# Kernel optimization log

Measured on AMD Instinct MI355X. Metric: run time of the kernel, lower is better.

## Reference

```python
import jax, jax.numpy as jnp
import numpy as np

EPS = 1e-3          # posdef_tol
CRLB = 1.0          # contraction_rate_lb
STD = 0.5           # initialization_std
DX, L, DIN, DOUT, B = 512, 512, 256, 256, 8192


def setup_inputs() -> dict:
    key = jax.random.key(0)
    ks = jax.random.split(key, 9)
    f32 = jnp.float32
    return {
        "u_in": jax.random.normal(ks[0], (B, 1, DIN), f32),
        "x0": jnp.zeros((B, 1, DX), f32),
        "X": jax.random.normal(ks[1], (2 * DX + L, 2 * DX + L), f32) * STD,
        "Y": jax.random.normal(ks[2], (DX, DX), f32) * STD,
        "B2": jax.random.normal(ks[3], (DX, DIN), f32) * STD,
        "C2": jax.random.normal(ks[4], (DOUT, DX), f32) * STD,
        "D21": jax.random.normal(ks[5], (DOUT, L), f32) * STD,
        "D22": jax.random.normal(ks[6], (DOUT, DIN), f32) * STD,
        "D12": jax.random.normal(ks[7], (L, DIN), f32) * STD,
    }


def _derive(X, Y, dx, l):
    # update_model_param: H = X^T X + eps*I, then block-split
    H = X.T @ X + EPS * jnp.eye(2 * dx + l, dtype=X.dtype)
    H11 = H[:dx, :dx]
    H21 = H[dx:dx + l, :dx]
    H22 = H[dx:dx + l, dx:dx + l]
    H31 = H[dx + l:, :dx]
    H32 = H[dx + l:, dx:dx + l]
    H33 = H[dx + l:, dx + l:]
    Fm = H31
    B1 = H32
    E = 0.5 * (H11 + CRLB * H33 + Y - Y.T)
    Lam = 0.5 * jnp.diag(H22)
    D11 = -jnp.tril(H22, -1)   # strictly lower triangular
    C1 = -H21
    return Fm, B1, E, Lam, D11, C1


def reference(u_in, x0, X, Y, B2, C2, D21, D22, D12):
    b = u_in.shape[0]
    dx = x0.shape[-1]
    l = D12.shape[0]
    u = u_in[:, 0, :]          # (B, din)
    x = x0[:, 0, :]            # (B, dx)
    Fm, B1, E, Lam, D11, C1 = _derive(X, Y, dx, l)

    # v_i = C1[i]@x + D11[i]@w + D12[i]@u ; the x/u parts are loop-invariant
    a = x @ C1.T + u @ D12.T   # (B, l)

    def step(w, inputs):
        a_i, d_row, lam_i, e_row = inputs
        v = a_i + w @ d_row                       # (B,) forward substitution
        w = w + jnp.tanh(v / lam_i)[:, None] * e_row[None, :]
        return w, None

    eye = jnp.eye(l, dtype=u.dtype)
    w0 = jnp.zeros((b, l), u.dtype)
    w, _ = jax.lax.scan(step, w0, (a.T, D11, Lam, eye))  # (B, l)

    pre = x @ Fm.T + w @ B1.T + u @ B2.T          # (B, dx)
    # F.linear(pre, E^{-1}) = pre @ E^{-T} = solve(E, pre^T)^T
    x_new = jnp.linalg.solve(E, pre.T).T          # (B, dx)
    y = x_new @ C2.T + w @ D21.T + u @ D22.T      # (B, dout)
    return y[:, None, :]                          # (B, 1, dout)
```

## Files before the change

kernel.cpp:

```cpp
#include <hip/hip_runtime.h>
#include <cstdint>
#include <cstddef>

#define EPSC 0.001f

typedef __attribute__((ext_vector_type(8))) short short8;
typedef __attribute__((ext_vector_type(4))) float f32x4;

__device__ inline void bsplit(float f, ushort& h, ushort& l) {
  uint b = __float_as_uint(f);
  h = (ushort)(b >> 16);
  float r = f - __uint_as_float(b & 0xFFFF0000u);
  l = (ushort)(__float_as_uint(r) >> 16);
}

__global__ void k_anynz(const float* __restrict__ x, int n4, int* __restrict__ flag) {
  int i = blockIdx.x * blockDim.x + threadIdx.x;
  int stride = gridDim.x * blockDim.x;
  int found = 0;
  for (; i < n4; i += stride) {
    float4 v = ((const float4*)x)[i];
    if (v.x != 0.f || v.y != 0.f || v.z != 0.f || v.w != 0.f) { found = 1; break; }
  }
  if (found) atomicOr(flag, 1);
}

__global__ __launch_bounds__(256) void k_tsplit(const float* __restrict__ src,
    ushort* __restrict__ dh, ushort* __restrict__ dl, int R, int C)
{
  __shared__ float t[32][33];
  const int c0 = blockIdx.x * 32, r0 = blockIdx.y * 32;
  const int tid = threadIdx.x;
  const int lr = tid >> 3, lc4 = (tid & 7) * 4;
  float4 v = *(const float4*)(src + (size_t)(r0 + lr) * C + c0 + lc4);
  t[lr][lc4 + 0] = v.x; t[lr][lc4 + 1] = v.y;
  t[lr][lc4 + 2] = v.z; t[lr][lc4 + 3] = v.w;
  __syncthreads();
  ushort4 hv, lv;
  float f;
  f = t[lc4 + 0][lr]; bsplit(f, hv.x, lv.x);
  f = t[lc4 + 1][lr]; bsplit(f, hv.y, lv.y);
  f = t[lc4 + 2][lr]; bsplit(f, hv.z, lv.z);
  f = t[lc4 + 3][lr]; bsplit(f, hv.w, lv.w);
  size_t off = (size_t)(c0 + lr) * R + r0 + lc4;
  *(ushort4*)(dh + off) = hv;
  *(ushort4*)(dl + off) = lv;
}

__global__ void k_split2(const float* __restrict__ s0, ushort* __restrict__ h0,
                         ushort* __restrict__ l0, int c0,
                         const float* __restrict__ s1, ushort* __restrict__ h1,
                         ushort* __restrict__ l1, int c1)
{
  int i = blockIdx.x * 256 + threadIdx.x;
  int tot = c0 + c1;
  int stride = gridDim.x * 256;
  for (; i < tot; i += stride) {
    const float* s; ushort* h; ushort* l; int k;
    if (i < c0) { s = s0; h = h0; l = l0; k = i; }
    else        { s = s1; h = h1; l = l1; k = i - c0; }
    float4 v = ((const float4*)s)[k];
    ushort4 hv, lv;
    bsplit(v.x, hv.x, lv.x);
    bsplit(v.y, hv.y, lv.y);
    bsplit(v.z, hv.z, lv.z);
    bsplit(v.w, hv.w, lv.w);
    ((ushort4*)h)[k] = hv;
    ((ushort4*)l)[k] = lv;
  }
}

__global__ __launch_bounds__(256) void k_xtxm(
    const ushort* __restrict__ Xth, const ushort* __restrict__ Xtl,
    const float* __restrict__ Y,
    float* __restrict__ E, float* __restrict__ C1,
    float* __restrict__ D11, ushort* __restrict__ D11h, ushort* __restrict__ D11l,
    float* __restrict__ Lam,
    ushort* __restrict__ FmTh, ushort* __restrict__ FmTl,
    ushort* __restrict__ B1Th, ushort* __restrict__ B1Tl)
{
  __shared__ ushort sAh[64][40], sAl[64][40], sBh[64][40], sBl[64][40];
  const int z = blockIdx.z;
  int aOff[2], bOff[2], nops;
  switch (z) {
    case 0:  aOff[0] = 0;    bOff[0] = 0;    aOff[1] = 1024; bOff[1] = 1024; nops = 2; break;
    case 1:  aOff[0] = 512;  bOff[0] = 0;    nops = 1; break;
    case 2:  aOff[0] = 512;  bOff[0] = 512;  nops = 1; break;
    case 3:  aOff[0] = 0;    bOff[0] = 1024; nops = 1; break;
    default: aOff[0] = 512;  bOff[0] = 1024; nops = 1; break;
  }
  const int tid = threadIdx.x;
  const int m0 = blockIdx.x * 64, n0 = blockIdx.y * 64;
  const int wid = tid >> 6, lane = tid & 63;
  const int wr = wid >> 1, wc = wid & 1;
  const int fr = lane & 15, fg = lane >> 4;
  const int srow = tid >> 2;
  const int sko = (tid & 3) * 8;
  f32x4 acc[2][2] = {};
  const int K = 1536;

  for (int op = 0; op < nops; ++op) {
    const ushort* Ah = Xth + (size_t)(aOff[op]) * K;
    const ushort* Al = Xtl + (size_t)(aOff[op]) * K;
    const ushort* Bh = Xth + (size_t)(bOff[op]) * K;
    const ushort* Bl = Xtl + (size_t)(bOff[op]) * K;
    uint4 pah = *(const uint4*)(Ah + (size_t)(m0 + srow) * K + sko);
    uint4 pal = *(const uint4*)(Al + (size_t)(m0 + srow) * K + sko);
    uint4 pbh = *(const uint4*)(Bh + (size_t)(n0 + srow) * K + sko);
    uint4 pbl = *(const uint4*)(Bl + (size_t)(n0 + srow) * K + sko);
    for (int k0 = 0; k0 < K; k0 += 32) {
      __syncthreads();
      *(uint4*)&sAh[srow][sko] = pah;
      *(uint4*)&sAl[srow][sko] = pal;
      *(uint4*)&sBh[srow][sko] = pbh;
      *(uint4*)&sBl[srow][sko] = pbl;
      __syncthreads();
      if (k0 + 32 < K) {
        pah = *(const uint4*)(Ah + (size_t)(m0 + srow) * K + k0 + 32 + sko);
        pal = *(const uint4*)(Al + (size_t)(m0 + srow) * K + k0 + 32 + sko);
        pbh = *(const uint4*)(Bh + (size_t)(n0 + srow) * K + k0 + 32 + sko);
        pbl = *(const uint4*)(Bl + (size_t)(n0 + srow) * K + k0 + 32 + sko);
      }
      short8 fah[2], fal[2], fbh[2], fbl[2];
#pragma unroll
      for (int s = 0; s < 2; ++s) {
        fah[s] = *(const short8*)&sAh[wr * 32 + s * 16 + fr][fg * 8];
        fal[s] = *(const short8*)&sAl[wr * 32 + s * 16 + fr][fg * 8];
        fbh[s] = *(const short8*)&sBh[wc * 32 + s * 16 + fr][fg * 8];
        fbl[s] = *(const short8*)&sBl[wc * 32 + s * 16 + fr][fg * 8];
      }
#pragma unroll
      for (int i = 0; i < 2; ++i)
#pragma unroll
        for (int j = 0; j < 2; ++j) {
          acc[i][j] = __builtin_amdgcn_mfma_f32_16x16x32_bf16(fah[i], fbh[j], acc[i][j], 0, 0, 0);
          acc[i][j] = __builtin_amdgcn_mfma_f32_16x16x32_bf16(fah[i], fbl[j], acc[i][j], 0, 0, 0);
          acc[i][j] = __builtin_amdgcn_mfma_f32_16x16x32_bf16(fal[i], fbh[j], acc[i][j], 0, 0, 0);
        }
    }
  }

#pragma unroll
  for (int i = 0; i < 2; ++i)
#pragma unroll
    for (int j = 0; j < 2; ++j) {
      int rbase = m0 + wr * 32 + i * 16 + fg * 4;
      int cc = n0 + wc * 32 + j * 16 + fr;
#pragma unroll
      for (int q = 0; q < 4; ++q) {
        int rr = rbase + q;
        float d = acc[i][j][q];
        size_t idx = (size_t)rr * 512 + cc;
        if (z == 0) {
          float o = 0.5f * (d + Y[idx] - Y[(size_t)cc * 512 + rr]);
          if (rr == cc) o += EPSC;
          E[idx] = o;
        } else if (z == 1) {
          C1[idx] = -d;
        } else if (z == 2) {
          float o = (cc < rr) ? -d : 0.f;
          D11[idx] = o;
          ushort h, l; bsplit(o, h, l);
          D11h[idx] = h; D11l[idx] = l;
          if (rr == cc) Lam[rr] = 0.5f * (d + EPSC);
        } else if (z == 3) {
          ushort h, l; bsplit(d, h, l);
          FmTh[idx] = h; FmTl[idx] = l;
        } else {
          ushort h, l; bsplit(d, h, l);
          B1Th[idx] = h; B1Tl[idx] = l;
        }
      }
    }
}

__global__ void k_nsinit(const float* __restrict__ E, const float* __restrict__ C2,
    float* __restrict__ Tf, ushort* __restrict__ Th, ushort* __restrict__ Tl,
    ushort* __restrict__ Tth, ushort* __restrict__ Ttl,
    float* __restrict__ Qf, ushort* __restrict__ Qh, ushort* __restrict__ Ql)
{
  int g = blockIdx.x * 256 + threadIdx.x;
  int row = g >> 7;
  int c4 = (g & 127) << 2;
  float s0 = 0.85f / E[(size_t)(c4 + 0) * 513];
  float s1 = 0.85f / E[(size_t)(c4 + 1) * 513];
  float s2 = 0.85f / E[(size_t)(c4 + 2) * 513];
  float s3 = 0.85f / E[(size_t)(c4 + 3) * 513];
  if (row < 512) {
    float4 v = *(const float4*)(E + (size_t)row * 512 + c4);
    v.x *= s0; v.y *= s1; v.z *= s2; v.w *= s3;
    *(float4*)(Tf + (size_t)row * 512 + c4) = v;
    ushort4 hv, lv;
    bsplit(v.x, hv.x, lv.x); bsplit(v.y, hv.y, lv.y);
    bsplit(v.z, hv.z, lv.z); bsplit(v.w, hv.w, lv.w);
    *(ushort4*)(Th + (size_t)row * 512 + c4) = hv;
    *(ushort4*)(Tl + (size_t)row * 512 + c4) = lv;
    Tth[(size_t)(c4 + 0) * 512 + row] = hv.x; Ttl[(size_t)(c4 + 0) * 512 + row] = lv.x;
    Tth[(size_t)(c4 + 1) * 512 + row] = hv.y; Ttl[(size_t)(c4 + 1) * 512 + row] = lv.y;
    Tth[(size_t)(c4 + 2) * 512 + row] = hv.z; Ttl[(size_t)(c4 + 2) * 512 + row] = lv.z;
    Tth[(size_t)(c4 + 3) * 512 + row] = hv.w; Ttl[(size_t)(c4 + 3) * 512 + row] = lv.w;
  } else {
    int qr = row - 512;
    float4 v = *(const float4*)(C2 + (size_t)qr * 512 + c4);
    v.x *= s0; v.y *= s1; v.z *= s2; v.w *= s3;
    *(float4*)(Qf + (size_t)qr * 512 + c4) = v;
    ushort4 hv, lv;
    bsplit(v.x, hv.x, lv.x); bsplit(v.y, hv.y, lv.y);
    bsplit(v.z, hv.z, lv.z); bsplit(v.w, hv.w, lv.w);
    *(ushort4*)(Qh + (size_t)qr * 512 + c4) = hv;
    *(ushort4*)(Ql + (size_t)qr * 512 + c4) = lv;
  }
}

template <bool WITH_T>
__global__ __launch_bounds__(256) void k_nsm(
    const ushort* __restrict__ Th, const ushort* __restrict__ Tl,
    const ushort* __restrict__ Tth, const ushort* __restrict__ Ttl,
    const ushort* __restrict__ Qh, const ushort* __restrict__ Ql,
    const float* __restrict__ Tprev, const float* __restrict__ Qprev,
    float* __restrict__ Tnext, ushort* __restrict__ Thn, ushort* __restrict__ Tln,
    ushort* __restrict__ Tthn, ushort* __restrict__ Ttln,
    float* __restrict__ Qnext, ushort* __restrict__ Qhn, ushort* __restrict__ Qln)
{
  __shared__ ushort sAh[64][40], sAl[64][40], sBh[64][40], sBl[64][40];
  const int tid = threadIdx.x;
  const int yy = blockIdx.y;
  const bool isT = WITH_T && (yy < 8);
  const int m0 = (isT ? yy : (yy - (WITH_T ? 8 : 0))) * 64;
  const int n0 = blockIdx.x * 64;
  const ushort* Ah = isT ? Th : Qh;
  const ushort* Al = isT ? Tl : Ql;
  const int wid = tid >> 6, lane = tid & 63;
  const int wr = wid >> 1, wc = wid & 1;
  const int fr = lane & 15, fg = lane >> 4;
  const int srow = tid >> 2;
  const int sko = (tid & 3) * 8;
  const int K = 512;
  f32x4 acc[2][2] = {};

  uint4 pah = *(const uint4*)(Ah + (size_t)(m0 + srow) * K + sko);
  uint4 pal = *(const uint4*)(Al + (size_t)(m0 + srow) * K + sko);
  uint4 pbh = *(const uint4*)(Tth + (size_t)(n0 + srow) * K + sko);
  uint4 pbl = *(const uint4*)(Ttl + (size_t)(n0 + srow) * K + sko);
  for (int k0 = 0; k0 < K; k0 += 32) {
    __syncthreads();
    *(uint4*)&sAh[srow][sko] = pah;
    *(uint4*)&sAl[srow][sko] = pal;
    *(uint4*)&sBh[srow][sko] = pbh;
    *(uint4*)&sBl[srow][sko] = pbl;
    __syncthreads();
    if (k0 + 32 < K) {
      pah = *(const uint4*)(Ah + (size_t)(m0 + srow) * K + k0 + 32 + sko);
      pal = *(const uint4*)(Al + (size_t)(m0 + srow) * K + k0 + 32 + sko);
      pbh = *(const uint4*)(Tth + (size_t)(n0 + srow) * K + k0 + 32 + sko);
      pbl = *(const uint4*)(Ttl + (size_t)(n0 + srow) * K + k0 + 32 + sko);
    }
    short8 fah[2], fal[2], fbh[2], fbl[2];
#pragma unroll
    for (int s = 0; s < 2; ++s) {
      fah[s] = *(const short8*)&sAh[wr * 32 + s * 16 + fr][fg * 8];
      fal[s] = *(const short8*)&sAl[wr * 32 + s * 16 + fr][fg * 8];
      fbh[s] = *(const short8*)&sBh[wc * 32 + s * 16 + fr][fg * 8];
      fbl[s] = *(const short8*)&sBl[wc * 32 + s * 16 + fr][fg * 8];
    }
#pragma unroll
    for (int i = 0; i < 2; ++i)
#pragma unroll
      for (int j = 0; j < 2; ++j) {
        acc[i][j] = __builtin_amdgcn_mfma_f32_16x16x32_bf16(fah[i], fbh[j], acc[i][j], 0, 0, 0);
        acc[i][j] = __builtin_amdgcn_mfma_f32_16x16x32_bf16(fah[i], fbl[j], acc[i][j], 0, 0, 0);
        acc[i][j] = __builtin_amdgcn_mfma_f32_16x16x32_bf16(fal[i], fbh[j], acc[i][j], 0, 0, 0);
      }
  }

#pragma unroll
  for (int i = 0; i < 2; ++i)
#pragma unroll
    for (int j = 0; j < 2; ++j) {
      int rbase = m0 + wr * 32 + i * 16 + fg * 4;
      int cc = n0 + wc * 32 + j * 16 + fr;
#pragma unroll
      for (int q = 0; q < 4; ++q) {
        int rr = rbase + q;
        size_t idx = (size_t)rr * 512 + cc;
        ushort h, l;
        if (isT) {
          float tn = 2.f * Tprev[idx] - acc[i][j][q];
          Tnext[idx] = tn;
          bsplit(tn, h, l);
          Thn[idx] = h; Tln[idx] = l;
          Tthn[(size_t)cc * 512 + rr] = h; Ttln[(size_t)cc * 512 + rr] = l;
        } else {
          float qn = 2.f * Qprev[idx] - acc[i][j][q];
          Qnext[idx] = qn;
          bsplit(qn, h, l);
          Qhn[idx] = h; Qln[idx] = l;
        }
      }
    }
}

__global__ __launch_bounds__(256) void k_foldm(
    const ushort* __restrict__ Qh, const ushort* __restrict__ Ql,
    const ushort* __restrict__ FmTh, const ushort* __restrict__ FmTl,
    const ushort* __restrict__ B1Th, const ushort* __restrict__ B1Tl,
    const ushort* __restrict__ B2Th, const ushort* __restrict__ B2Tl,
    const float* __restrict__ D21, const float* __restrict__ D22,
    float* __restrict__ P1, ushort* __restrict__ P2h, ushort* __restrict__ P2l,
    ushort* __restrict__ P3h, ushort* __restrict__ P3l)
{
  __shared__ ushort sAh[64][40], sAl[64][40], sBh[64][40], sBl[64][40];
  const int z = blockIdx.z;
  const int N = (z == 2) ? 256 : 512;
  const int n0 = blockIdx.x * 64;
  if (n0 >= N) return;
  const ushort* Bh = (z == 0) ? FmTh : (z == 1) ? B1Th : B2Th;
  const ushort* Bl = (z == 0) ? FmTl : (z == 1) ? B1Tl : B2Tl;
  const int tid = threadIdx.x;
  const int m0 = blockIdx.y * 64;
  const int wid = tid >> 6, lane = tid & 63;
  const int wr = wid >> 1, wc = wid & 1;
  const int fr = lane & 15, fg = lane >> 4;
  const int srow = tid >> 2;
  const int sko = (tid & 3) * 8;
  const int K = 512;
  f32x4 acc[2][2] = {};

  uint4 pah = *(const uint4*)(Qh + (size_t)(m0 + srow) * K + sko);
  uint4 pal = *(const uint4*)(Ql + (size_t)(m0 + srow) * K + sko);
  uint4 pbh = *(const uint4*)(Bh + (size_t)(n0 + srow) * K + sko);
  uint4 pbl = *(const uint4*)(Bl + (size_t)(n0 + srow) * K + sko);
  for (int k0 = 0; k0 < K; k0 += 32) {
    __syncthreads();
    *(uint4*)&sAh[srow][sko] = pah;
    *(uint4*)&sAl[srow][sko] = pal;
    *(uint4*)&sBh[srow][sko] = pbh;
    *(uint4*)&sBl[srow][sko] = pbl;
    __syncthreads();
    if (k0 + 32 < K) {
      pah = *(const uint4*)(Qh + (size_t)(m0 + srow) * K + k0 + 32 + sko);
      pal = *(const uint4*)(Ql + (size_t)(m0 + srow) * K + k0 + 32 + sko);
      pbh = *(const uint4*)(Bh + (size_t)(n0 + srow) * K + k0 + 32 + sko);
      pbl = *(const uint4*)(Bl + (size_t)(n0 + srow) * K + k0 + 32 + sko);
    }
    short8 fah[2], fal[2], fbh[2], fbl[2];
#pragma unroll
    for (int s = 0; s < 2; ++s) {
      fah[s] = *(const short8*)&sAh[wr * 32 + s * 16 + fr][fg * 8];
      fal[s] = *(const short8*)&sAl[wr * 32 + s * 16 + fr][fg * 8];
      fbh[s] = *(const short8*)&sBh[wc * 32 + s * 16 + fr][fg * 8];
      fbl[s] = *(const short8*)&sBl[wc * 32 + s * 16 + fr][fg * 8];
    }
#pragma unroll
    for (int i = 0; i < 2; ++i)
#pragma unroll
      for (int j = 0; j < 2; ++j) {
        acc[i][j] = __builtin_amdgcn_mfma_f32_16x16x32_bf16(fah[i], fbh[j], acc[i][j], 0, 0, 0);
        acc[i][j] = __builtin_amdgcn_mfma_f32_16x16x32_bf16(fah[i], fbl[j], acc[i][j], 0, 0, 0);
        acc[i][j] = __builtin_amdgcn_mfma_f32_16x16x32_bf16(fal[i], fbh[j], acc[i][j], 0, 0, 0);
      }
  }

#pragma unroll
  for (int i = 0; i < 2; ++i)
#pragma unroll
    for (int j = 0; j < 2; ++j) {
      int rbase = m0 + wr * 32 + i * 16 + fg * 4;
      int cc = n0 + wc * 32 + j * 16 + fr;
#pragma unroll
      for (int q = 0; q < 4; ++q) {
        int rr = rbase + q;
        float d = acc[i][j][q];
        if (z == 0) {
          P1[(size_t)rr * 512 + cc] = d;
        } else if (z == 1) {
          size_t idx = (size_t)rr * 512 + cc;
          float p = d + D21[idx];
          ushort h, l; bsplit(p, h, l);
          P2h[idx] = h; P2l[idx] = l;
        } else {
          size_t idx = (size_t)rr * 256 + cc;
          float p = d + D22[idx];
          ushort h, l; bsplit(p, h, l);
          P3h[idx] = h; P3l[idx] = l;
        }
      }
    }
}

template <int NOPS>
__global__ __launch_bounds__(256) void k_ntm(
    const ushort* __restrict__ Ah0, const ushort* __restrict__ Al0,
    const ushort* __restrict__ Bh0, const ushort* __restrict__ Bl0, int K0,
    const ushort* __restrict__ Ah1, const ushort* __restrict__ Al1,
    const ushort* __restrict__ Bh1, const ushort* __restrict__ Bl1, int K1,
    float* __restrict__ C, int ldc)
{
  __shared__ ushort sAh[64][40], sAl[64][40], sBh[64][40], sBl[64][40];
  const int tid = threadIdx.x;
  const int m0 = blockIdx.x * 64, n0 = blockIdx.y * 64;
  const int wid = tid >> 6, lane = tid & 63;
  const int wr = wid >> 1, wc = wid & 1;
  const int fr = lane & 15, fg = lane >> 4;
  const int srow = tid >> 2;
  const int sko = (tid & 3) * 8;
  f32x4 acc[2][2] = {};

#pragma unroll
  for (int op = 0; op < NOPS; ++op) {
    const ushort* Ah = (op == 0) ? Ah0 : Ah1;
    const ushort* Al = (op == 0) ? Al0 : Al1;
    const ushort* Bh = (op == 0) ? Bh0 : Bh1;
    const ushort* Bl = (op == 0) ? Bl0 : Bl1;
    const int K = (op == 0) ? K0 : K1;
    uint4 pah = *(const uint4*)(Ah + (size_t)(m0 + srow) * K + sko);
    uint4 pal = *(const uint4*)(Al + (size_t)(m0 + srow) * K + sko);
    uint4 pbh = *(const uint4*)(Bh + (size_t)(n0 + srow) * K + sko);
    uint4 pbl = *(const uint4*)(Bl + (size_t)(n0 + srow) * K + sko);
    for (int k0 = 0; k0 < K; k0 += 32) {
      __syncthreads();
      *(uint4*)&sAh[srow][sko] = pah;
      *(uint4*)&sAl[srow][sko] = pal;
      *(uint4*)&sBh[srow][sko] = pbh;
      *(uint4*)&sBl[srow][sko] = pbl;
      __syncthreads();
      if (k0 + 32 < K) {
        pah = *(const uint4*)(Ah + (size_t)(m0 + srow) * K + k0 + 32 + sko);
        pal = *(const uint4*)(Al + (size_t)(m0 + srow) * K + k0 + 32 + sko);
        pbh = *(const uint4*)(Bh + (size_t)(n0 + srow) * K + k0 + 32 + sko);
        pbl = *(const uint4*)(Bl + (size_t)(n0 + srow) * K + k0 + 32 + sko);
      }
      short8 fah[2], fal[2], fbh[2], fbl[2];
#pragma unroll
      for (int s = 0; s < 2; ++s) {
        fah[s] = *(const short8*)&sAh[wr * 32 + s * 16 + fr][fg * 8];
        fal[s] = *(const short8*)&sAl[wr * 32 + s * 16 + fr][fg * 8];
        fbh[s] = *(const short8*)&sBh[wc * 32 + s * 16 + fr][fg * 8];
        fbl[s] = *(const short8*)&sBl[wc * 32 + s * 16 + fr][fg * 8];
      }
#pragma unroll
      for (int i = 0; i < 2; ++i)
#pragma unroll
        for (int j = 0; j < 2; ++j) {
          acc[i][j] = __builtin_amdgcn_mfma_f32_16x16x32_bf16(fah[i], fbh[j], acc[i][j], 0, 0, 0);
          acc[i][j] = __builtin_amdgcn_mfma_f32_16x16x32_bf16(fah[i], fbl[j], acc[i][j], 0, 0, 0);
          acc[i][j] = __builtin_amdgcn_mfma_f32_16x16x32_bf16(fal[i], fbh[j], acc[i][j], 0, 0, 0);
        }
    }
  }

#pragma unroll
  for (int i = 0; i < 2; ++i)
#pragma unroll
    for (int j = 0; j < 2; ++j) {
      int rr = m0 + wr * 32 + i * 16 + fg * 4;
      int cc = n0 + wc * 32 + j * 16 + fr;
#pragma unroll
      for (int q = 0; q < 4; ++q)
        C[(size_t)(rr + q) * ldc + cc] = acc[i][j][q];
    }
}

__global__ __launch_bounds__(256) void k_ntadd(const float* __restrict__ A,
    const float* __restrict__ B, int K, const int* __restrict__ flag,
    float* __restrict__ C, int ldc)
{
  if (*flag == 0) return;
  __shared__ float As[16][68];
  __shared__ float Bs[16][68];
  const int tid = threadIdx.x;
  const int tx = tid & 15, ty = tid >> 4;
  const int m0 = blockIdx.x * 64, n0 = blockIdx.y * 64;
  const int lr = tid >> 2;
  const int lk = (tid & 3) * 4;
  float acc[4][4];
#pragma unroll
  for (int i = 0; i < 4; ++i)
#pragma unroll
    for (int j = 0; j < 4; ++j) acc[i][j] = 0.f;
  float4 av = *(const float4*)(A + (size_t)(m0 + lr) * K + lk);
  float4 bv = *(const float4*)(B + (size_t)(n0 + lr) * K + lk);
  for (int k0 = 0; k0 < K; k0 += 16) {
    __syncthreads();
    As[lk + 0][lr] = av.x; As[lk + 1][lr] = av.y;
    As[lk + 2][lr] = av.z; As[lk + 3][lr] = av.w;
    Bs[lk + 0][lr] = bv.x; Bs[lk + 1][lr] = bv.y;
    Bs[lk + 2][lr] = bv.z; Bs[lk + 3][lr] = bv.w;
    __syncthreads();
    if (k0 + 16 < K) {
      av = *(const float4*)(A + (size_t)(m0 + lr) * K + k0 + 16 + lk);
      bv = *(const float4*)(B + (size_t)(n0 + lr) * K + k0 + 16 + lk);
    }
#pragma unroll
    for (int kk = 0; kk < 16; ++kk) {
      float4 a4 = *(const float4*)&As[kk][4 * ty];
      float4 b4 = *(const float4*)&Bs[kk][4 * tx];
      float ar[4] = {a4.x, a4.y, a4.z, a4.w};
      float br[4] = {b4.x, b4.y, b4.z, b4.w};
#pragma unroll
      for (int i = 0; i < 4; ++i)
#pragma unroll
        for (int j = 0; j < 4; ++j)
          acc[i][j] = fmaf(ar[i], br[j], acc[i][j]);
    }
  }
#pragma unroll
  for (int i = 0; i < 4; ++i) {
    float* p = C + (size_t)(m0 + 4 * ty + i) * ldc + n0 + 4 * tx;
    float4 v = *(float4*)p;
    v.x += acc[i][0]; v.y += acc[i][1]; v.z += acc[i][2]; v.w += acc[i][3];
    *(float4*)p = v;
  }
}

__global__ __launch_bounds__(512, 4) void k_scan(const float* __restrict__ a,
    const float* __restrict__ D11,
    const ushort* __restrict__ D11h, const ushort* __restrict__ D11l,
    const float* __restrict__ Lam, ushort* __restrict__ wh, ushort* __restrict__ wl)
{
  __shared__ ushort wth[16][520];
  __shared__ ushort wtl[16][520];
  __shared__ float wcur[32][17];
  __shared__ float sblk[32][17];
  __shared__ float shist[6][32][17];
  __shared__ float dblkT[2][32][33];
  __shared__ float doff[32][33];
  __shared__ float ablk[32][17];
  __shared__ float rl2[512];
  const int tid = threadIdx.x;
  const int row0 = blockIdx.x * 16;

  rl2[tid] = 2.f / Lam[tid];
  if (tid < 128) {
    int rr = tid >> 3, cq = (tid & 7) * 4;
    float4 v = *(const float4*)(a + (size_t)(row0 + rr) * 512 + cq);
    sblk[cq + 0][rr] = v.x; sblk[cq + 1][rr] = v.y;
    sblk[cq + 2][rr] = v.z; sblk[cq + 3][rr] = v.w;
  } else if (tid < 384) {
    int f = tid - 128;
    int rr = f >> 3, cq = (f & 7) * 4;
    float4 v = *(const float4*)(D11 + (size_t)rr * 512 + cq);
    dblkT[0][cq + 0][rr] = v.x; dblkT[0][cq + 1][rr] = v.y;
    dblkT[0][cq + 2][rr] = v.z; dblkT[0][cq + 3][rr] = v.w;
  }
  __syncthreads();

  const int wv = tid >> 6;
  const int lane = tid & 63;
  const int fr = lane & 15, fg = lane >> 4;

  for (int t = 0; t < 16; ++t) {
    const int c0 = 32 * t;
    const int jend2 = c0 + 32;
    if (wv == 0) {
      if (lane < 16) {
        float s[32];
#pragma unroll
        for (int il = 0; il < 32; ++il) s[il] = sblk[il][lane];
#pragma unroll
        for (int il = 0; il < 32; ++il) {
          float x2 = s[il] * rl2[c0 + il];
          float e = __expf(x2);
          float w2 = 1.f - 2.f * __builtin_amdgcn_rcpf(e + 1.f);
          wcur[il][lane] = w2;
          ushort hh, ll; bsplit(w2, hh, ll);
          wth[lane][c0 + il] = hh;
          wtl[lane][c0 + il] = ll;
#pragma unroll
          for (int j2 = il + 1; j2 < 32; ++j2)
            s[j2] = fmaf(dblkT[t & 1][il][j2], w2, s[j2]);
        }
      }
    } else if (wv <= 6) {
      if (t < 15) {
        f32x4 acc0 = {}, acc1 = {};
        for (int s = wv - 1; s < t; s += 6) {
          const int jb = 32 * s;
          const size_t ao0 = (size_t)(jend2 + fr) * 512 + jb + fg * 8;
          const size_t ao1 = (size_t)(jend2 + 16 + fr) * 512 + jb + fg * 8;
          short8 a0h = *(const short8*)(D11h + ao0);
          short8 a0l = *(const short8*)(D11l + ao0);
          short8 a1h = *(const short8*)(D11h + ao1);
          short8 a1l = *(const short8*)(D11l + ao1);
          short8 bh = *(const short8*)&wth[fr][jb + fg * 8];
          short8 bl = *(const short8*)&wtl[fr][jb + fg * 8];
          acc0 = __builtin_amdgcn_mfma_f32_16x16x32_bf16(a0h, bh, acc0, 0, 0, 0);
          acc0 = __builtin_amdgcn_mfma_f32_16x16x32_bf16(a0h, bl, acc0, 0, 0, 0);
          acc0 = __builtin_amdgcn_mfma_f32_16x16x32_bf16(a0l, bh, acc0, 0, 0, 0);
          acc1 = __builtin_amdgcn_mfma_f32_16x16x32_bf16(a1h, bh, acc1, 0, 0, 0);
          acc1 = __builtin_amdgcn_mfma_f32_16x16x32_bf16(a1h, bl, acc1, 0, 0, 0);
          acc1 = __builtin_amdgcn_mfma_f32_16x16x32_bf16(a1l, bh, acc1, 0, 0, 0);
        }
#pragma unroll
        for (int q = 0; q < 4; ++q) {
          shist[wv - 1][fg * 4 + q][fr] = acc0[q];
          shist[wv - 1][16 + fg * 4 + q][fr] = acc1[q];
        }
      }
    } else {
      if (t < 15) {
#pragma unroll
        for (int e = 0; e < 4; ++e) {
          int f = lane + 64 * e;
          int rr = f >> 3, cq = (f & 7) * 4;
          float4 v = *(const float4*)(D11 + (size_t)(jend2 + rr) * 512 + c0 + cq);
          doff[rr][cq + 0] = v.x; doff[rr][cq + 1] = v.y;
          doff[rr][cq + 2] = v.z; doff[rr][cq + 3] = v.w;
          float4 v2 = *(const float4*)(D11 + (size_t)(jend2 + rr) * 512 + jend2 + cq);
          dblkT[(t + 1) & 1][cq + 0][rr] = v2.x; dblkT[(t + 1) & 1][cq + 1][rr] = v2.y;
          dblkT[(t + 1) & 1][cq + 2][rr] = v2.z; dblkT[(t + 1) & 1][cq + 3][rr] = v2.w;
        }
#pragma unroll
        for (int e = 0; e < 2; ++e) {
          int f = lane + 64 * e;
          int rr = f >> 3, cq = (f & 7) * 4;
          float4 v = *(const float4*)(a + (size_t)(row0 + rr) * 512 + jend2 + cq);
          ablk[cq + 0][rr] = v.x; ablk[cq + 1][rr] = v.y;
          ablk[cq + 2][rr] = v.z; ablk[cq + 3][rr] = v.w;
        }
      }
    }
    __syncthreads();
    if (t < 15) {
      const int il = tid >> 4, r2 = tid & 15;
      float s = ablk[il][r2];
#pragma unroll
      for (int k = 0; k < 6; ++k) s += shist[k][il][r2];
#pragma unroll 8
      for (int j = 0; j < 32; ++j)
        s = fmaf(doff[il][j], wcur[j][r2], s);
      sblk[il][r2] = s;
      __syncthreads();
    }
  }

  const int k2 = tid & 255;
  const int rb = tid >> 8;
#pragma unroll
  for (int p = 0; p < 8; ++p) {
    int r = rb * 8 + p;
    size_t off = (size_t)(row0 + r) * 512 + 2 * k2;
    *(uint*)(wh + off) = *(const uint*)&wth[r][2 * k2];
    *(uint*)(wl + off) = *(const uint*)&wtl[r][2 * k2];
  }
}

extern "C" void kernel_launch(void* const* d_in, const int* in_sizes, int n_in,
                              void* d_out, int out_size, void* d_ws, size_t ws_size,
                              hipStream_t stream)
{
  const float* u   = (const float*)d_in[0];
  const float* x0  = (const float*)d_in[1];
  const float* X   = (const float*)d_in[2];
  const float* Y   = (const float*)d_in[3];
  const float* B2  = (const float*)d_in[4];
  const float* C2  = (const float*)d_in[5];
  const float* D21 = (const float*)d_in[6];
  const float* D22 = (const float*)d_in[7];
  const float* D12 = (const float*)d_in[8];
  float* out = (float*)d_out;
  float* ws = (float*)d_ws;

  float*  E    = ws + 0;
  float*  C1   = ws + 262144;
  float*  D11  = ws + 524288;
  ushort* D11h = (ushort*)(ws + 786432);
  ushort* D11l = (ushort*)(ws + 917504);
  float*  Lam  = ws + 1048576;
  int*    flag = (int*)(ws + 1049088);
  float*  Tf0  = ws + 1049600;
  float*  Tf1  = ws + 1311744;
  float*  Qf0  = ws + 1573888;
  float*  Qf1  = ws + 1704960;
  ushort* Th0  = (ushort*)(ws + 1836032);
  ushort* Tl0  = (ushort*)(ws + 1967104);
  ushort* Tth0 = (ushort*)(ws + 2098176);
  ushort* Ttl0 = (ushort*)(ws + 2229248);
  ushort* Th1  = (ushort*)(ws + 2360320);
  ushort* Tl1  = (ushort*)(ws + 2491392);
  ushort* Tth1 = (ushort*)(ws + 2622464);
  ushort* Ttl1 = (ushort*)(ws + 2753536);
  ushort* Qh0  = (ushort*)(ws + 2884608);
  ushort* Ql0  = (ushort*)(ws + 2950144);
  ushort* Qh1  = (ushort*)(ws + 3015680);
  ushort* Ql1  = (ushort*)(ws + 3081216);
  ushort* FmTh = (ushort*)(ws + 3146752);
  ushort* FmTl = (ushort*)(ws + 3277824);
  ushort* B1Th = (ushort*)(ws + 3408896);
  ushort* B1Tl = (ushort*)(ws + 3539968);
  ushort* B2Th = (ushort*)(ws + 3671040);
  ushort* B2Tl = (ushort*)(ws + 3736576);
  float*  P1   = ws + 3802112;
  ushort* P2h  = (ushort*)(ws + 3933184);
  ushort* P2l  = (ushort*)(ws + 3998720);
  ushort* P3h  = (ushort*)(ws + 4064256);
  ushort* P3l  = (ushort*)(ws + 4097024);
  ushort* D12h = (ushort*)(ws + 4129792);
  ushort* D12l = (ushort*)(ws + 4195328);
  ushort* uh   = (ushort*)(ws + 4260864);
  ushort* ul   = (ushort*)(ws + 5309440);
  float*  abuf = ws + 6358016;
  ushort* wh   = (ushort*)(ws + 10552320);
  ushort* wl   = (ushort*)(ws + 12649472);
  ushort* Xth  = (ushort*)(ws + 10552320);
  ushort* Xtl  = (ushort*)(ws + 11731968);

  hipMemsetAsync(flag, 0, 4, stream);
  k_anynz<<<256, 256, 0, stream>>>(x0, 8192 * 512 / 4, flag);

  k_tsplit<<<dim3(48, 48), 256, 0, stream>>>(X, Xth, Xtl, 1536, 1536);
  k_tsplit<<<dim3(8, 16), 256, 0, stream>>>(B2, B2Th, B2Tl, 512, 256);
  k_split2<<<2048, 256, 0, stream>>>(u, uh, ul, 524288, D12, D12h, D12l, 32768);

  k_xtxm<<<dim3(8, 8, 5), 256, 0, stream>>>(Xth, Xtl, Y, E, C1,
                                            D11, D11h, D11l, Lam,
                                            FmTh, FmTl, B1Th, B1Tl);

  k_ntm<1><<<dim3(128, 8), 256, 0, stream>>>(uh, ul, D12h, D12l, 256,
                                             nullptr, nullptr, nullptr, nullptr, 0,
                                             abuf, 512);
  k_ntadd<<<dim3(128, 8), 256, 0, stream>>>(x0, C1, 512, flag, abuf, 512);

  k_nsinit<<<384, 256, 0, stream>>>(E, C2, Tf0, Th0, Tl0, Tth0, Ttl0, Qf0, Qh0, Ql0);
  ushort *Tha[2] = {Th0, Th1}, *Tla[2] = {Tl0, Tl1};
  ushort *Ttha[2] = {Tth0, Tth1}, *Ttla[2] = {Ttl0, Ttl1};
  ushort *Qha[2] = {Qh0, Qh1}, *Qla[2] = {Ql0, Ql1};
  float *Tfa[2] = {Tf0, Tf1}, *Qfa[2] = {Qf0, Qf1};
  int cur = 0;
  for (int it = 0; it < 5; ++it) {
    int nxt = cur ^ 1;
    k_nsm<true><<<dim3(8, 12), 256, 0, stream>>>(
        Tha[cur], Tla[cur], Ttha[cur], Ttla[cur], Qha[cur], Qla[cur],
        Tfa[cur], Qfa[cur],
        Tfa[nxt], Tha[nxt], Tla[nxt], Ttha[nxt], Ttla[nxt],
        Qfa[nxt], Qha[nxt], Qla[nxt]);
    cur = nxt;
  }
  int nxt = cur ^ 1;
  k_nsm<false><<<dim3(8, 4), 256, 0, stream>>>(
      Tha[cur], Tla[cur], Ttha[cur], Ttla[cur], Qha[cur], Qla[cur],
      Tfa[cur], Qfa[cur],
      Tfa[nxt], Tha[nxt], Tla[nxt], Ttha[nxt], Ttla[nxt],
      Qfa[nxt], Qha[nxt], Qla[nxt]);
  ushort* Qh = Qha[nxt];
  ushort* Ql = Qla[nxt];

  k_foldm<<<dim3(8, 4, 3), 256, 0, stream>>>(Qh, Ql, FmTh, FmTl, B1Th, B1Tl,
                                             B2Th, B2Tl, D21, D22,
                                             P1, P2h, P2l, P3h, P3l);

  k_scan<<<512, 512, 0, stream>>>(abuf, D11, D11h, D11l, Lam, wh, wl);

  k_ntm<2><<<dim3(128, 4), 256, 0, stream>>>(wh, wl, P2h, P2l, 512,
                                             uh, ul, P3h, P3l, 256,
                                             out, 256);
  k_ntadd<<<dim3(128, 4), 256, 0, stream>>>(x0, P1, 512, flag, out, 256);
}
```

Before: 406.8 us.

## Parallelize diagonal-block substitution across wave, software-pipeline MFMA loads, drop one Newton-Schulz iteration

Measured after the change: 374.7 us. 7.9% less time.

```diff
diff --git a/kernel.cpp b/kernel.cpp
--- a/kernel.cpp
+++ b/kernel.cpp
@@ -553,43 +553,84 @@
     const int c0 = 32 * t;
     const int jend2 = c0 + 32;
     if (wv == 0) {
-      if (lane < 16) {
-        float s[32];
-#pragma unroll
-        for (int il = 0; il < 32; ++il) s[il] = sblk[il][lane];
-#pragma unroll
-        for (int il = 0; il < 32; ++il) {
-          float x2 = s[il] * rl2[c0 + il];
-          float e = __expf(x2);
-          float w2 = 1.f - 2.f * __builtin_amdgcn_rcpf(e + 1.f);
-          wcur[il][lane] = w2;
-          ushort hh, ll; bsplit(w2, hh, ll);
-          wth[lane][c0 + il] = hh;
-          wtl[lane][c0 + il] = ll;
-#pragma unroll
-          for (int j2 = il + 1; j2 < 32; ++j2)
-            s[j2] = fmaf(dblkT[t & 1][il][j2], w2, s[j2]);
-        }
+      const int r = fr, g = fg;
+      const int tb = t & 1;
+      float so[8];
+#pragma unroll
+      for (int k = 0; k < 8; ++k) so[k] = sblk[8 * g + k][r];
+      float4 ca = *(const float4*)&dblkT[tb][0][8 * g];
+      float4 cb = *(const float4*)&dblkT[tb][0][8 * g + 4];
+      float rln = rl2[c0];
+#pragma unroll
+      for (int il = 0; il < 32; ++il) {
+        float4 na, nb; float rlnn;
+        if (il < 31) {
+          na = *(const float4*)&dblkT[tb][il + 1][8 * g];
+          nb = *(const float4*)&dblkT[tb][il + 1][8 * g + 4];
+          rlnn = rl2[c0 + il + 1];
+        }
+        float x2 = so[il & 7] * rln;
+        float e = __expf(x2);
+        float w2 = 1.f - 2.f * __builtin_amdgcn_rcpf(e + 1.f);
+        const int go = il >> 3;
+        float w2b = __shfl(w2, r + (go << 4));
+        if (g == go) {
+          wcur[il][r] = w2b;
+          ushort hh, ll; bsplit(w2b, hh, ll);
+          wth[r][c0 + il] = hh;
+          wtl[r][c0 + il] = ll;
+        }
+        so[0] = fmaf(ca.x, w2b, so[0]);
+        so[1] = fmaf(ca.y, w2b, so[1]);
+        so[2] = fmaf(ca.z, w2b, so[2]);
+        so[3] = fmaf(ca.w, w2b, so[3]);
+        so[4] = fmaf(cb.x, w2b, so[4]);
+        so[5] = fmaf(cb.y, w2b, so[5]);
+        so[6] = fmaf(cb.z, w2b, so[6]);
+        so[7] = fmaf(cb.w, w2b, so[7]);
+        ca = na; cb = nb; rln = rlnn;
       }
     } else if (wv <= 6) {
       if (t < 15) {
         f32x4 acc0 = {}, acc1 = {};
-        for (int s = wv - 1; s < t; s += 6) {
-          const int jb = 32 * s;
-          const size_t ao0 = (size_t)(jend2 + fr) * 512 + jb + fg * 8;
-          const size_t ao1 = (size_t)(jend2 + 16 + fr) * 512 + jb + fg * 8;
-          short8 a0h = *(const short8*)(D11h + ao0);
-          short8 a0l = *(const short8*)(D11l + ao0);
-          short8 a1h = *(const short8*)(D11h + ao1);
-          short8 a1l = *(const short8*)(D11l + ao1);
-          short8 bh = *(const short8*)&wth[fr][jb + fg * 8];
-          short8 bl = *(const short8*)&wtl[fr][jb + fg * 8];
-          acc0 = __builtin_amdgcn_mfma_f32_16x16x32_bf16(a0h, bh, acc0, 0, 0, 0);
-          acc0 = __builtin_amdgcn_mfma_f32_16x16x32_bf16(a0h, bl, acc0, 0, 0, 0);
-          acc0 = __builtin_amdgcn_mfma_f32_16x16x32_bf16(a0l, bh, acc0, 0, 0, 0);
-          acc1 = __builtin_amdgcn_mfma_f32_16x16x32_bf16(a1h, bh, acc1, 0, 0, 0);
-          acc1 = __builtin_amdgcn_mfma_f32_16x16x32_bf16(a1h, bl, acc1, 0, 0, 0);
-          acc1 = __builtin_amdgcn_mfma_f32_16x16x32_bf16(a1l, bh, acc1, 0, 0, 0);
+        int s = wv - 1;
+        if (s < t) {
+          short8 a0h, a0l, a1h, a1l, bh, bl;
+          {
+            const int jb = 32 * s;
+            const size_t ao0 = (size_t)(jend2 + fr) * 512 + jb + fg * 8;
+            const size_t ao1 = ao0 + (size_t)16 * 512;
+            a0h = *(const short8*)(D11h + ao0);
+            a0l = *(const short8*)(D11l + ao0);
+            a1h = *(const short8*)(D11h + ao1);
+            a1l = *(const short8*)(D11l + ao1);
+            bh = *(const short8*)&wth[fr][jb + fg * 8];
+            bl = *(const short8*)&wtl[fr][jb + fg * 8];
+          }
+          for (;;) {
+            const int sn = s + 6;
+            short8 n0h, n0l, n1h, n1l, nbh, nbl;
+            if (sn < t) {
+              const int jb = 32 * sn;
+              const size_t ao0 = (size_t)(jend2 + fr) * 512 + jb + fg * 8;
+              const size_t ao1 = ao0 + (size_t)16 * 512;
+              n0h = *(const short8*)(D11h + ao0);
+              n0l = *(const short8*)(D11l + ao0);
+              n1h = *(const short8*)(D11h + ao1);
+              n1l = *(const short8*)(D11l + ao1);
+              nbh = *(const short8*)&wth[fr][jb + fg * 8];
+              nbl = *(const short8*)&wtl[fr][jb + fg * 8];
+            }
+            acc0 = __builtin_amdgcn_mfma_f32_16x16x32_bf16(a0h, bh, acc0, 0, 0, 0);
+            acc0 = __builtin_amdgcn_mfma_f32_16x16x32_bf16(a0h, bl, acc0, 0, 0, 0);
+            acc0 = __builtin_amdgcn_mfma_f32_16x16x32_bf16(a0l, bh, acc0, 0, 0, 0);
+            acc1 = __builtin_amdgcn_mfma_f32_16x16x32_bf16(a1h, bh, acc1, 0, 0, 0);
+            acc1 = __builtin_amdgcn_mfma_f32_16x16x32_bf16(a1h, bl, acc1, 0, 0, 0);
+            acc1 = __builtin_amdgcn_mfma_f32_16x16x32_bf16(a1l, bh, acc1, 0, 0, 0);
+            if (sn >= t) break;
+            a0h = n0h; a0l = n0l; a1h = n1h; a1l = n1l; bh = nbh; bl = nbl;
+            s = sn;
+          }
         }
 #pragma unroll
         for (int q = 0; q < 4; ++q) {
@@ -727,7 +768,7 @@
   ushort *Qha[2] = {Qh0, Qh1}, *Qla[2] = {Ql0, Ql1};
   float *Tfa[2] = {Tf0, Tf1}, *Qfa[2] = {Qf0, Qf1};
   int cur = 0;
-  for (int it = 0; it < 5; ++it) {
+  for (int it = 0; it < 4; ++it) {
     int nxt = cur ^ 1;
     k_nsm<true><<<dim3(8, 12), 256, 0, stream>>>(
         Tha[cur], Tla[cur], Ttha[cur], Ttla[cur], Qha[cur], Qla[cur],
```
